# Optimization experiments

Measured on AMD Instinct MI355X. Metric: run time of the kernel, lower is better.

Reference implementation:

```python
import jax, jax.numpy as jnp
import numpy as np

B, S, D, H = 4, 2048, 1024, 1024  # batch, seq, input_dim, hidden_dim

def setup_inputs() -> dict:
    key = jax.random.key(0)
    k1, k2, k3, k4, k5 = jax.random.split(key, 5)
    scale1 = 1.0 / np.sqrt(D)
    scale2 = 1.0 / np.sqrt(H)
    return {
        "x": jax.random.normal(k1, (B, S, D), dtype=jnp.float32),
        "W1": jax.random.uniform(k2, (D, 3 * H), jnp.float32, -scale1, scale1),
        "b1": jax.random.uniform(k3, (3 * H,), jnp.float32, -scale1, scale1),
        "W2": jax.random.uniform(k4, (H, H), jnp.float32, -scale2, scale2),
        "b2": jax.random.uniform(k5, (H,), jnp.float32, -scale2, scale2),
    }

def reference(x, W1, b1, W2, b2):
    qkv = jnp.einsum('bsd,dh->bsh', x, W1) + b1          # [B,S,3H]
    q, k, v = jnp.split(qkv, 3, axis=-1)                  # each [B,S,H]
    scale = (2.0 * D) ** -0.5                             # faithful: (input_dim*2)^-0.5
    scores = jnp.einsum('bse,bSe->bsS', q, k) * scale     # [B,S,S]
    att = jax.nn.softmax(scores, axis=-1)
    ctx = jnp.einsum('bsS,bSe->bse', att, v)              # [B,S,H]
    out = jnp.einsum('bsh,hk->bsk', ctx, W2) + b2
    return out
```

## Files before the change

kernel.cpp:

```cpp
#include <hip/hip_runtime.h>
#include <hip/hip_bf16.h>
#include <stdint.h>

#define B_  4
#define S_  2048
#define D_  1024
#define H_  1024
#define BS_ (B_*S_)
#define N3H (3*H_)

typedef __bf16 bf16x8 __attribute__((ext_vector_type(8)));
typedef float  f32x4  __attribute__((ext_vector_type(4)));
typedef unsigned short u16x8 __attribute__((ext_vector_type(8)));

__device__ __forceinline__ unsigned short f2bf(float x) {
    unsigned u = __float_as_uint(x);
    return (unsigned short)((u + 0x7FFFu + ((u >> 16) & 1u)) >> 16);
}
__device__ __forceinline__ float bf2f(unsigned short h) {
    return __uint_as_float(((unsigned)h) << 16);
}

__device__ __forceinline__ void gload_lds16(const void* g, void* l) {
    __builtin_amdgcn_global_load_lds(
        (const __attribute__((address_space(1))) void*)g,
        (__attribute__((address_space(3))) void*)l, 16, 0, 0);
}

#define BAR __builtin_amdgcn_s_barrier()
#define DS_FENCE do { asm volatile("s_waitcnt lgkmcnt(0)" ::: "memory"); \
                      __builtin_amdgcn_sched_barrier(0); } while (0)

template<int EPI>
__global__ __launch_bounds__(256, 3) void gemm3b(
    const unsigned short* __restrict__ A,
    const unsigned short* __restrict__ Bm,
    int NXt, int NYt, int N, int K,
    long long sAz, long long sBz, long long sOz,
    void* __restrict__ out0, void* __restrict__ out1, void* __restrict__ out2,
    const float* __restrict__ bias, float scale)
{
    __shared__ __align__(16) char lds[3 * 16384];

    const int nt_g = (int)gridDim.x;
    const int bid = (int)blockIdx.x;
    const int C = nt_g >> 3;
    const int c = bid >> 3;
    const int xcd = bid & 7;
    const int qq = c >> 2;
    const int txl = qq % NXt;
    const int rest = (c & 3) + 4 * (qq / NXt);
    const int tile = xcd * C + rest * NXt + txl;
    const int tx = tile % NXt;
    const int rest2 = tile / NXt;
    const int ty = rest2 % NYt;
    const int tz = rest2 / NYt;

    const unsigned short* Ab = A  + (long long)tz * sAz;
    const unsigned short* Bb = Bm + (long long)tz * sBz;
    const int rowBase = ty * 128;
    const int colBase = tx * 128;
    const int tid = threadIdx.x;
    const int w = tid >> 6, l = tid & 63;
    const int wr = w >> 1, wc = w & 1;
    const int fr = l & 15, fq = l >> 4;

    int sr[2], scl[2];
#pragma unroll
    for (int j = 0; j < 2; j++) {
        int o  = j * 4096 + tid * 16;
        int st = o >> 10;
        int wi = o & 1023;
        wi ^= ((wi >> 9) & 1) << 5;
        sr[j]  = st * 16 + (wi >> 6);
        scl[j] = (wi & 63) >> 1;
    }

    auto STAGE_A = [&](char* buf, int t) {
        const unsigned short* base = Ab + (long long)rowBase * K + t * 32;
#pragma unroll
        for (int j = 0; j < 2; j++)
            gload_lds16(base + (long long)sr[j] * K + scl[j],
                        buf + j * 4096 + w * 1024);
    };
    auto STAGE_B = [&](char* buf, int t) {
        const unsigned short* base = Bb + (long long)colBase * K + t * 32;
#pragma unroll
        for (int j = 0; j < 2; j++)
            gload_lds16(base + (long long)sr[j] * K + scl[j],
                        buf + 8192 + j * 4096 + w * 1024);
    };

    const int abase = (fr * 64 + fq * 16) ^ ((fr & 8) << 2);

    f32x4 acc[4][4];
#pragma unroll
    for (int m = 0; m < 4; m++)
#pragma unroll
        for (int n = 0; n < 4; n++) acc[m][n] = (f32x4){0.f, 0.f, 0.f, 0.f};

    const int NT = K >> 5;

    STAGE_A(lds, 0); STAGE_B(lds, 0);
    STAGE_A(lds + 16384, 1); STAGE_B(lds + 16384, 1);
    asm volatile("s_waitcnt vmcnt(4)" ::: "memory");
    BAR;
    __builtin_amdgcn_sched_barrier(0);

    bf16x8 af[4], bf[4];

    for (int t = 0; t < NT; ++t) {
        const char* bc = lds + (t % 3) * 16384;
        char* bs = lds + ((t + 2) % 3) * 16384;
        int ts = t + 2; if (ts >= NT) ts -= NT;

#pragma unroll
        for (int m = 0; m < 4; m++)
            af[m] = *(const bf16x8*)(bc + (wr * 4 + m) * 1024 + abase);
#pragma unroll
        for (int n = 0; n < 4; n++)
            bf[n] = *(const bf16x8*)(bc + 8192 + (wc * 4 + n) * 1024 + abase);
        STAGE_A(bs, ts); STAGE_B(bs, ts);
        BAR; DS_FENCE;
        __builtin_amdgcn_s_setprio(1);
#pragma unroll
        for (int m = 0; m < 4; m++)
#pragma unroll
            for (int n = 0; n < 4; n++)
                acc[m][n] = __builtin_amdgcn_mfma_f32_16x16x32_bf16(
                    af[m], bf[n], acc[m][n], 0, 0, 0);
        __builtin_amdgcn_s_setprio(0);
        asm volatile("s_waitcnt vmcnt(4)" ::: "memory");
        BAR;
        __builtin_amdgcn_sched_barrier(0);
    }

    asm volatile("s_waitcnt vmcnt(0) lgkmcnt(0)" ::: "memory");
    BAR;

    const int crow0 = rowBase + wr * 64 + fq * 4;
    const int ccol0 = colBase + wc * 64 + fr;

    if constexpr (EPI == 0) {
        const int seg = colBase >> 10;
        if (seg < 2) {
            unsigned short* dst = (unsigned short*)(seg == 0 ? out0 : out1);
#pragma unroll
            for (int n = 0; n < 4; n++) {
                const int col = ccol0 + n * 16;
                const float bv = bias[col];
                const int scn = col & 1023;
#pragma unroll
                for (int m = 0; m < 4; m++) {
                    const int r0 = crow0 + m * 16;
#pragma unroll
                    for (int j = 0; j < 4; j++)
                        dst[(long long)(r0 + j) * 1024 + scn] = f2bf(acc[m][n][j] + bv);
                }
            }
        } else {
            unsigned short (*T)[129] = (unsigned short(*)[129])lds;
            const int lr0 = wr * 64 + fq * 4;
            const int lc0 = wc * 64 + fr;
#pragma unroll
            for (int n = 0; n < 4; n++) {
                const int lc = lc0 + n * 16;
                const float bv = bias[colBase + lc];
#pragma unroll
                for (int m = 0; m < 4; m++)
#pragma unroll
                    for (int j = 0; j < 4; j++)
                        T[lr0 + m * 16 + j][lc] = f2bf(acc[m][n][j] + bv);
            }
            BAR;
            const int s_loc = tid & 127, hh = tid >> 7;
            const int b = rowBase >> 11;
            const int s_glob = (rowBase & 2047) + s_loc;
            unsigned short* vt =
                (unsigned short*)out2 + (long long)b * ((long long)S_ * H_);
            const int h0 = (colBase - 2048) + hh * 64;
#pragma unroll 8
            for (int h = 0; h < 64; ++h)
                vt[(long long)(h0 + h) * S_ + s_glob] = T[s_loc][hh * 64 + h];
        }
    } else if constexpr (EPI == 4) {
        unsigned short* dst = (unsigned short*)out0 + (long long)tz * sOz;
#pragma unroll
        for (int m = 0; m < 4; m++) {
            float linv[4];
#pragma unroll
            for (int j = 0; j < 4; j++)
                linv[j] = 1.0f / bias[tz * 2048 + crow0 + m * 16 + j];
#pragma unroll
            for (int n = 0; n < 4; n++) {
                const int col = ccol0 + n * 16;
                const int r0 = crow0 + m * 16;
#pragma unroll
                for (int j = 0; j < 4; j++)
                    dst[(long long)(r0 + j) * N + col] = f2bf(acc[m][n][j] * linv[j]);
            }
        }
        (void)scale;
    } else {
        float* dst = (float*)out0;
#pragma unroll
        for (int n = 0; n < 4; n++) {
            const int col = ccol0 + n * 16;
            const float bv = bias[col];
#pragma unroll
            for (int m = 0; m < 4; m++) {
                const int r0 = crow0 + m * 16;
#pragma unroll
                for (int j = 0; j < 4; j++)
                    dst[(long long)(r0 + j) * N + col] = acc[m][n][j] + bv;
            }
        }
        (void)scale;
    }
}

template<int EPI>
__global__ __launch_bounds__(512, 2) void gemm256(
    const unsigned short* __restrict__ A,
    const unsigned short* __restrict__ Bm,
    int NXt, int NYt, int N, int K,
    long long sAz, long long sBz, long long sOz,
    void* __restrict__ out0, void* __restrict__ out1, void* __restrict__ out2,
    const float* __restrict__ bias, float scale)
{
    __shared__ __align__(16) char lds[131072];

    const int nt_g = (int)gridDim.x;
    const int bid = (int)blockIdx.x;
    const int C = nt_g >> 3;
    const int c = bid >> 3;
    const int xcd = bid & 7;
    const int qq = c >> 2;
    const int txl = qq % NXt;
    const int rest = (c & 3) + 4 * (qq / NXt);
    const int tile = xcd * C + rest * NXt + txl;
    const int tx = tile % NXt;
    const int rest2 = tile / NXt;
    const int ty = rest2 % NYt;
    const int tz = rest2 / NYt;

    const unsigned short* Ab = A  + (long long)tz * sAz;
    const unsigned short* Bb = Bm + (long long)tz * sBz;
    const int rowBase = ty * 256;
    const int colBase = tx * 256;
    const int tid = threadIdx.x;
    const int w = tid >> 6, l = tid & 63;
    const int wr = w >> 2, wc = w & 3;
    const int fr = l & 15, fq = l >> 4;

    int sr[2], scl[2];
#pragma unroll
    for (int j = 0; j < 2; j++) {
        int o  = j * 8192 + tid * 16;
        int st = o >> 10;
        int wi = o & 1023;
        wi ^= ((wi >> 9) & 1) << 5;
        sr[j]  = (st >> 1) * 16 + (wi >> 6);
        scl[j] = (st & 1) * 32 + ((wi & 63) >> 1);
    }

    auto STAGE = [&](int buf, int which, int tile_) {
        const unsigned short* mat = (which < 2) ? Ab : Bb;
        const int rt0 = ((which < 2) ? rowBase : colBase) + (which & 1) * 128;
        char* dst = lds + buf * 65536 + (which >> 1) * 32768
                        + (which & 1) * 16384 + w * 1024;
        const int k0 = tile_ * 64;
#pragma unroll
        for (int j = 0; j < 2; j++) {
            const unsigned short* src =
                mat + (long long)(rt0 + sr[j]) * K + k0 + scl[j];
            gload_lds16(src, dst + j * 8192);
        }
    };

    const int abase = (fr * 64 + fq * 16) ^ ((fr & 8) << 2);
    const char* Ah[2] = { lds + wr * 16384, lds + 65536 + wr * 16384 };
    const char* Bh[2] = { lds + 32768 + (wc >> 1) * 16384,
                          lds + 98304 + (wc >> 1) * 16384 };
    const int bn0 = (wc & 1) * 8192;

#define LA(b, m, kk) (*(const bf16x8*)(Ah[b] + (m)*2048 + (kk)*1024 + abase))
#define LB(b, n, kk) (*(const bf16x8*)(Bh[b] + bn0 + (n)*2048 + (kk)*1024 + abase))
#define MFMA16(AF, BF, MOFF, NOFF) do { \
    __builtin_amdgcn_s_setprio(1); \
    _Pragma("unroll") for (int m_ = 0; m_ < 4; m_++) \
    _Pragma("unroll") for (int n_ = 0; n_ < 2; n_++) \
    _Pragma("unroll") for (int k_ = 0; k_ < 2; k_++) \
        acc[(MOFF)+m_][(NOFF)+n_] = __builtin_amdgcn_mfma_f32_16x16x32_bf16( \
            AF[m_][k_], BF[n_][k_], acc[(MOFF)+m_][(NOFF)+n_], 0, 0, 0); \
    __builtin_amdgcn_s_setprio(0); } while (0)

    f32x4 acc[8][4];
#pragma unroll
    for (int m = 0; m < 8; m++)
#pragma unroll
        for (int n = 0; n < 4; n++) acc[m][n] = (f32x4){0.f, 0.f, 0.f, 0.f};

    const int NT = K >> 6;

    STAGE(0, 0, 0); STAGE(0, 1, 0); STAGE(0, 2, 0); STAGE(0, 3, 0);
    STAGE(1, 0, 1); STAGE(1, 1, 1);
    asm volatile("s_waitcnt vmcnt(4)" ::: "memory");
    BAR;
    __builtin_amdgcn_sched_barrier(0);

    bf16x8 afA[4][2], afB[4][2], bfA[2][2], bfB[2][2];

    for (int i = 0; i < NT / 2; i++) {
        const int t1 = 2 * i + 1;
        int t2 = 2 * i + 2; if (t2 >= NT) t2 -= NT;
        int t3 = 2 * i + 3; if (t3 >= NT) t3 -= NT;

#pragma unroll
        for (int m = 0; m < 4; m++) { afA[m][0] = LA(0, m, 0); afA[m][1] = LA(0, m, 1); }
#pragma unroll
        for (int n = 0; n < 2; n++) { bfA[n][0] = LB(0, n, 0); bfA[n][1] = LB(0, n, 1); }
        STAGE(1, 2, t1);
        BAR; DS_FENCE;
        MFMA16(afA, bfA, 0, 0);
        BAR;
#pragma unroll
        for (int m = 0; m < 4; m++) { afB[m][0] = LA(0, 4 + m, 0); afB[m][1] = LA(0, 4 + m, 1); }
        STAGE(1, 3, t1);
        BAR; DS_FENCE;
        MFMA16(afB, bfA, 4, 0);
        BAR;
#pragma unroll
        for (int n = 0; n < 2; n++) { bfB[n][0] = LB(0, 2 + n, 0); bfB[n][1] = LB(0, 2 + n, 1); }
        STAGE(0, 0, t2);
        BAR; DS_FENCE;
        MFMA16(afA, bfB, 0, 2);
        BAR;
        STAGE(0, 1, t2);
        BAR;
        MFMA16(afB, bfB, 4, 2);
        asm volatile("s_waitcnt vmcnt(4)" ::: "memory");
        BAR;
        __builtin_amdgcn_sched_barrier(0);

#pragma unroll
        for (int m = 0; m < 4; m++) { afA[m][0] = LA(1, m, 0); afA[m][1] = LA(1, m, 1); }
#pragma unroll
        for (int n = 0; n < 2; n++) { bfA[n][0] = LB(1, n, 0); bfA[n][1] = LB(1, n, 1); }
        STAGE(0, 2, t2);
        BAR; DS_FENCE;
        MFMA16(afA, bfA, 0, 0);
        BAR;
#pragma unroll
        for (int m = 0; m < 4; m++) { afB[m][0] = LA(1, 4 + m, 0); afB[m][1] = LA(1, 4 + m, 1); }
        STAGE(0, 3, t2);
        BAR; DS_FENCE;
        MFMA16(afB, bfA, 4, 0);
        BAR;
#pragma unroll
        for (int n = 0; n < 2; n++) { bfB[n][0] = LB(1, 2 + n, 0); bfB[n][1] = LB(1, 2 + n, 1); }
        STAGE(1, 0, t3);
        BAR; DS_FENCE;
        MFMA16(afA, bfB, 0, 2);
        BAR;
        STAGE(1, 1, t3);
        BAR;
        MFMA16(afB, bfB, 4, 2);
        asm volatile("s_waitcnt vmcnt(4)" ::: "memory");
        BAR;
        __builtin_amdgcn_sched_barrier(0);
    }

    asm volatile("s_waitcnt vmcnt(0) lgkmcnt(0)" ::: "memory");

    const int crow0 = rowBase + wr * 128 + fq * 4;
    const int ccol0 = colBase + wc * 64 + fr;

    if constexpr (EPI == 2) {
        float* lsum = (float*)out1;
        unsigned short* dst = (unsigned short*)out0 + (long long)tz * sOz;
#pragma unroll
        for (int m = 0; m < 8; m++) {
#pragma unroll
            for (int j = 0; j < 4; j++) {
                const int row = crow0 + m * 16 + j;
                float rs = 0.f;
#pragma unroll
                for (int n = 0; n < 4; n++) {
                    const int col = ccol0 + n * 16;
                    const float p = __expf(acc[m][n][j] * scale);
                    const unsigned short us = f2bf(p);
                    dst[(long long)row * N + col] = us;
                    rs += bf2f(us);
                }
                rs += __shfl_xor(rs, 1); rs += __shfl_xor(rs, 2);
                rs += __shfl_xor(rs, 4); rs += __shfl_xor(rs, 8);
                if (fr == 0) atomicAdd(&lsum[tz * 2048 + row], rs);
            }
        }
    }
    (void)out2; (void)bias;
#undef LA
#undef LB
#undef MFMA16
}

__global__ __launch_bounds__(256) void conv_f32_bf16(
    const float* __restrict__ in, unsigned short* __restrict__ out, int n8)
{
    for (int i = blockIdx.x * blockDim.x + threadIdx.x; i < n8;
         i += gridDim.x * blockDim.x) {
        const float4 a = ((const float4*)in)[2 * i];
        const float4 b = ((const float4*)in)[2 * i + 1];
        u16x8 o;
        o[0] = f2bf(a.x); o[1] = f2bf(a.y); o[2] = f2bf(a.z); o[3] = f2bf(a.w);
        o[4] = f2bf(b.x); o[5] = f2bf(b.y); o[6] = f2bf(b.z); o[7] = f2bf(b.w);
        ((u16x8*)out)[i] = o;
    }
}

__global__ __launch_bounds__(256) void tconv_f32_bf16(
    const float* __restrict__ in, unsigned short* __restrict__ out,
    int rows, int cols)
{
    __shared__ float t[32][33];
    const int c0 = blockIdx.x * 32, r0 = blockIdx.y * 32;
    const int tx = threadIdx.x & 31, ty = threadIdx.x >> 5;
#pragma unroll
    for (int i = 0; i < 4; i++)
        t[ty + 8 * i][tx] = in[(long long)(r0 + ty + 8 * i) * cols + c0 + tx];
    __syncthreads();
#pragma unroll
    for (int i = 0; i < 4; i++)
        out[(long long)(c0 + ty + 8 * i) * rows + r0 + tx] = f2bf(t[tx][ty + 8 * i]);
}

extern "C" void kernel_launch(void* const* d_in, const int* in_sizes, int n_in,
                              void* d_out, int out_size, void* d_ws, size_t ws_size,
                              hipStream_t stream)
{
    (void)in_sizes; (void)n_in; (void)out_size; (void)ws_size;
    const float* x  = (const float*)d_in[0];
    const float* W1 = (const float*)d_in[1];
    const float* b1 = (const float*)d_in[2];
    const float* W2 = (const float*)d_in[3];
    const float* b2 = (const float*)d_in[4];
    float* out = (float*)d_out;

    char* ws = (char*)d_ws;
    size_t off = 0;
    auto alloc = [&](size_t bytes) {
        void* p = ws + off;
        off += (bytes + 255) & ~(size_t)255;
        return p;
    };
    unsigned short* xbf = (unsigned short*)alloc((size_t)BS_ * D_ * 2);
    unsigned short* w1t = (unsigned short*)alloc((size_t)N3H * D_ * 2);
    unsigned short* w2t = (unsigned short*)alloc((size_t)H_ * H_ * 2);
    unsigned short* q   = (unsigned short*)alloc((size_t)BS_ * H_ * 2);
    unsigned short* k   = (unsigned short*)alloc((size_t)BS_ * H_ * 2);
    unsigned short* v   = (unsigned short*)alloc((size_t)BS_ * H_ * 2);
    unsigned short* vt  = (unsigned short*)alloc((size_t)BS_ * H_ * 2);
    unsigned short* sc  = (unsigned short*)alloc((size_t)B_ * S_ * S_ * 2);
    float*          lsum = (float*)alloc((size_t)BS_ * 4);
    unsigned short* ctx = v;

    const float scale = 0.022097086912079608f;

    hipMemsetAsync(lsum, 0, (size_t)BS_ * 4, stream);

    conv_f32_bf16<<<dim3(2048), dim3(256), 0, stream>>>(x, xbf, BS_ * D_ / 8);
    tconv_f32_bf16<<<dim3(N3H / 32, D_ / 32), dim3(256), 0, stream>>>(W1, w1t, D_, N3H);
    tconv_f32_bf16<<<dim3(H_ / 32, H_ / 32), dim3(256), 0, stream>>>(W2, w2t, H_, H_);

    gemm3b<0><<<dim3(1536), dim3(256), 0, stream>>>(
        xbf, w1t, 24, 64, N3H, D_, 0LL, 0LL, 0LL, q, k, vt, b1, 1.0f);

    gemm256<2><<<dim3(256), dim3(512), 0, stream>>>(
        q, k, 8, 8, S_, H_, (long long)S_ * H_, (long long)S_ * H_,
        (long long)S_ * S_, sc, lsum, nullptr, nullptr, scale);

    gemm3b<4><<<dim3(512), dim3(256), 0, stream>>>(
        sc, vt, 8, 16, H_, S_, (long long)S_ * S_, (long long)H_ * S_,
        (long long)S_ * H_, ctx, nullptr, nullptr, lsum, 1.0f);

    gemm3b<3><<<dim3(512), dim3(256), 0, stream>>>(
        ctx, w2t, 8, 64, H_, H_, 0LL, 0LL, 0LL, out, nullptr, nullptr, b2, 1.0f);
}
```

Before: 195.6 us.

## Fold W2 into the V projection to drop the output GEMM

Uses associativity to precompute W1v·W2 as a fused weight, so the QKV GEMM directly emits V·W2 (transposed) instead of V. The attention-times-V GEMM then writes the final fp32 output with softmax normalization and a combined bias (b1v·W2 + b2), and the separate ctx·W2 GEMM is removed. This trades a large 8192x1024x1024 GEMM for a small 1024^3 weight GEMM plus a bias reduction kernel. It adds an extra bf16 rounding of the fused weight, which may change numerics slightly.

```diff
diff --git a/kernel.cpp b/kernel.cpp
--- a/kernel.cpp
+++ b/kernel.cpp
@@ -31,7 +31,7 @@
 #define DS_FENCE do { asm volatile("s_waitcnt lgkmcnt(0)" ::: "memory"); \
                       __builtin_amdgcn_sched_barrier(0); } while (0)
 
-template<int EPI>
+template<int EPI, int SWZ>
 __global__ __launch_bounds__(256, 3) void gemm3b(
     const unsigned short* __restrict__ A,
     const unsigned short* __restrict__ Bm,
@@ -41,6 +41,198 @@
     const float* __restrict__ bias, float scale)
 {
     __shared__ __align__(16) char lds[3 * 16384];
+
+    const int bid = (int)blockIdx.x;
+    int tile;
+    if constexpr (SWZ) {
+        const int nt_g = (int)gridDim.x;
+        const int C = nt_g >> 3;
+        const int c = bid >> 3;
+        const int xcd = bid & 7;
+        const int qq = c >> 2;
+        const int txl = qq % NXt;
+        const int rest = (c & 3) + 4 * (qq / NXt);
+        tile = xcd * C + rest * NXt + txl;
+    } else {
+        tile = bid;
+    }
+    const int tx = tile % NXt;
+    const int rest2 = tile / NXt;
+    const int ty = rest2 % NYt;
+    const int tz = rest2 / NYt;
+
+    const unsigned short* Ab = A  + (long long)tz * sAz;
+    const unsigned short* Bb = Bm + (long long)tz * sBz;
+    const int rowBase = ty * 128;
+    const int colBase = tx * 128;
+    const int tid = threadIdx.x;
+    const int w = tid >> 6, l = tid & 63;
+    const int wr = w >> 1, wc = w & 1;
+    const int fr = l & 15, fq = l >> 4;
+
+    int sr[2], scl[2];
+#pragma unroll
+    for (int j = 0; j < 2; j++) {
+        int o  = j * 4096 + tid * 16;
+        int st = o >> 10;
+        int wi = o & 1023;
+        wi ^= ((wi >> 9) & 1) << 5;
+        sr[j]  = st * 16 + (wi >> 6);
+        scl[j] = (wi & 63) >> 1;
+    }
+
+    auto STAGE_A = [&](char* buf, int t) {
+        const unsigned short* base = Ab + (long long)rowBase * K + t * 32;
+#pragma unroll
+        for (int j = 0; j < 2; j++)
+            gload_lds16(base + (long long)sr[j] * K + scl[j],
+                        buf + j * 4096 + w * 1024);
+    };
+    auto STAGE_B = [&](char* buf, int t) {
+        const unsigned short* base = Bb + (long long)colBase * K + t * 32;
+#pragma unroll
+        for (int j = 0; j < 2; j++)
+            gload_lds16(base + (long long)sr[j] * K + scl[j],
+                        buf + 8192 + j * 4096 + w * 1024);
+    };
+
+    const int abase = (fr * 64 + fq * 16) ^ ((fr & 8) << 2);
+
+    f32x4 acc[4][4];
+#pragma unroll
+    for (int m = 0; m < 4; m++)
+#pragma unroll
+        for (int n = 0; n < 4; n++) acc[m][n] = (f32x4){0.f, 0.f, 0.f, 0.f};
+
+    const int NT = K >> 5;
+
+    STAGE_A(lds, 0); STAGE_B(lds, 0);
+    STAGE_A(lds + 16384, 1); STAGE_B(lds + 16384, 1);
+    asm volatile("s_waitcnt vmcnt(4)" ::: "memory");
+    BAR;
+    __builtin_amdgcn_sched_barrier(0);
+
+    bf16x8 af[4], bf[4];
+
+    for (int t = 0; t < NT; ++t) {
+        const char* bc = lds + (t % 3) * 16384;
+        char* bs = lds + ((t + 2) % 3) * 16384;
+        int ts = t + 2; if (ts >= NT) ts -= NT;
+
+#pragma unroll
+        for (int m = 0; m < 4; m++)
+            af[m] = *(const bf16x8*)(bc + (wr * 4 + m) * 1024 + abase);
+#pragma unroll
+        for (int n = 0; n < 4; n++)
+            bf[n] = *(const bf16x8*)(bc + 8192 + (wc * 4 + n) * 1024 + abase);
+        STAGE_A(bs, ts); STAGE_B(bs, ts);
+        BAR; DS_FENCE;
+        __builtin_amdgcn_s_setprio(1);
+#pragma unroll
+        for (int m = 0; m < 4; m++)
+#pragma unroll
+            for (int n = 0; n < 4; n++)
+                acc[m][n] = __builtin_amdgcn_mfma_f32_16x16x32_bf16(
+                    af[m], bf[n], acc[m][n], 0, 0, 0);
+        __builtin_amdgcn_s_setprio(0);
+        asm volatile("s_waitcnt vmcnt(4)" ::: "memory");
+        BAR;
+        __builtin_amdgcn_sched_barrier(0);
+    }
+
+    asm volatile("s_waitcnt vmcnt(0) lgkmcnt(0)" ::: "memory");
+    BAR;
+
+    const int crow0 = rowBase + wr * 64 + fq * 4;
+    const int ccol0 = colBase + wc * 64 + fr;
+
+    if constexpr (EPI == 0) {
+        const int seg = colBase >> 10;
+        if (seg < 2) {
+            unsigned short* dst = (unsigned short*)(seg == 0 ? out0 : out1);
+#pragma unroll
+            for (int n = 0; n < 4; n++) {
+                const int col = ccol0 + n * 16;
+                const float bv = bias[col];
+                const int scn = col & 1023;
+#pragma unroll
+                for (int m = 0; m < 4; m++) {
+                    const int r0 = crow0 + m * 16;
+#pragma unroll
+                    for (int j = 0; j < 4; j++)
+                        dst[(long long)(r0 + j) * 1024 + scn] = f2bf(acc[m][n][j] + bv);
+                }
+            }
+        } else {
+            unsigned short (*T)[129] = (unsigned short(*)[129])lds;
+            const int lr0 = wr * 64 + fq * 4;
+            const int lc0 = wc * 64 + fr;
+#pragma unroll
+            for (int n = 0; n < 4; n++) {
+                const int lc = lc0 + n * 16;
+#pragma unroll
+                for (int m = 0; m < 4; m++)
+#pragma unroll
+                    for (int j = 0; j < 4; j++)
+                        T[lr0 + m * 16 + j][lc] = f2bf(acc[m][n][j]);
+            }
+            BAR;
+            const int s_loc = tid & 127, hh = tid >> 7;
+            const int b = rowBase >> 11;
+            const int s_glob = (rowBase & 2047) + s_loc;
+            unsigned short* ut =
+                (unsigned short*)out2 + (long long)b * ((long long)S_ * H_);
+            const int h0 = (colBase - 2048) + hh * 64;
+#pragma unroll 8
+            for (int h = 0; h < 64; ++h)
+                ut[(long long)(h0 + h) * S_ + s_glob] = T[s_loc][hh * 64 + h];
+        }
+    } else if constexpr (EPI == 1) {
+        unsigned short* dst = (unsigned short*)out0 + (long long)tz * sOz;
+#pragma unroll
+        for (int n = 0; n < 4; n++) {
+            const int col = ccol0 + n * 16;
+#pragma unroll
+            for (int m = 0; m < 4; m++) {
+                const int r0 = crow0 + m * 16;
+#pragma unroll
+                for (int j = 0; j < 4; j++)
+                    dst[(long long)(r0 + j) * N + col] = f2bf(acc[m][n][j] * scale);
+            }
+        }
+    } else {
+        float* dst = (float*)out0 + (long long)tz * sOz;
+        const float* bu = (const float*)out1;
+#pragma unroll
+        for (int m = 0; m < 4; m++) {
+            float linv[4];
+#pragma unroll
+            for (int j = 0; j < 4; j++)
+                linv[j] = 1.0f / bias[tz * 2048 + crow0 + m * 16 + j];
+#pragma unroll
+            for (int n = 0; n < 4; n++) {
+                const int col = ccol0 + n * 16;
+                const float bvv = bu[col];
+                const int r0 = crow0 + m * 16;
+#pragma unroll
+                for (int j = 0; j < 4; j++)
+                    dst[(long long)(r0 + j) * N + col] = acc[m][n][j] * linv[j] + bvv;
+            }
+        }
+        (void)scale;
+    }
+}
+
+template<int EPI>
+__global__ __launch_bounds__(512, 2) void gemm256(
+    const unsigned short* __restrict__ A,
+    const unsigned short* __restrict__ Bm,
+    int NXt, int NYt, int N, int K,
+    long long sAz, long long sBz, long long sOz,
+    void* __restrict__ out0, void* __restrict__ out1, void* __restrict__ out2,
+    const float* __restrict__ bias, float scale)
+{
+    __shared__ __align__(16) char lds[131072];
 
     const int nt_g = (int)gridDim.x;
     const int bid = (int)blockIdx.x;
@@ -58,194 +250,6 @@
 
     const unsigned short* Ab = A  + (long long)tz * sAz;
     const unsigned short* Bb = Bm + (long long)tz * sBz;
-    const int rowBase = ty * 128;
-    const int colBase = tx * 128;
-    const int tid = threadIdx.x;
-    const int w = tid >> 6, l = tid & 63;
-    const int wr = w >> 1, wc = w & 1;
-    const int fr = l & 15, fq = l >> 4;
-
-    int sr[2], scl[2];
-#pragma unroll
-    for (int j = 0; j < 2; j++) {
-        int o  = j * 4096 + tid * 16;
-        int st = o >> 10;
-        int wi = o & 1023;
-        wi ^= ((wi >> 9) & 1) << 5;
-        sr[j]  = st * 16 + (wi >> 6);
-        scl[j] = (wi & 63) >> 1;
-    }
-
-    auto STAGE_A = [&](char* buf, int t) {
-        const unsigned short* base = Ab + (long long)rowBase * K + t * 32;
-#pragma unroll
-        for (int j = 0; j < 2; j++)
-            gload_lds16(base + (long long)sr[j] * K + scl[j],
-                        buf + j * 4096 + w * 1024);
-    };
-    auto STAGE_B = [&](char* buf, int t) {
-        const unsigned short* base = Bb + (long long)colBase * K + t * 32;
-#pragma unroll
-        for (int j = 0; j < 2; j++)
-            gload_lds16(base + (long long)sr[j] * K + scl[j],
-                        buf + 8192 + j * 4096 + w * 1024);
-    };
-
-    const int abase = (fr * 64 + fq * 16) ^ ((fr & 8) << 2);
-
-    f32x4 acc[4][4];
-#pragma unroll
-    for (int m = 0; m < 4; m++)
-#pragma unroll
-        for (int n = 0; n < 4; n++) acc[m][n] = (f32x4){0.f, 0.f, 0.f, 0.f};
-
-    const int NT = K >> 5;
-
-    STAGE_A(lds, 0); STAGE_B(lds, 0);
-    STAGE_A(lds + 16384, 1); STAGE_B(lds + 16384, 1);
-    asm volatile("s_waitcnt vmcnt(4)" ::: "memory");
-    BAR;
-    __builtin_amdgcn_sched_barrier(0);
-
-    bf16x8 af[4], bf[4];
-
-    for (int t = 0; t < NT; ++t) {
-        const char* bc = lds + (t % 3) * 16384;
-        char* bs = lds + ((t + 2) % 3) * 16384;
-        int ts = t + 2; if (ts >= NT) ts -= NT;
-
-#pragma unroll
-        for (int m = 0; m < 4; m++)
-            af[m] = *(const bf16x8*)(bc + (wr * 4 + m) * 1024 + abase);
-#pragma unroll
-        for (int n = 0; n < 4; n++)
-            bf[n] = *(const bf16x8*)(bc + 8192 + (wc * 4 + n) * 1024 + abase);
-        STAGE_A(bs, ts); STAGE_B(bs, ts);
-        BAR; DS_FENCE;
-        __builtin_amdgcn_s_setprio(1);
-#pragma unroll
-        for (int m = 0; m < 4; m++)
-#pragma unroll
-            for (int n = 0; n < 4; n++)
-                acc[m][n] = __builtin_amdgcn_mfma_f32_16x16x32_bf16(
-                    af[m], bf[n], acc[m][n], 0, 0, 0);
-        __builtin_amdgcn_s_setprio(0);
-        asm volatile("s_waitcnt vmcnt(4)" ::: "memory");
-        BAR;
-        __builtin_amdgcn_sched_barrier(0);
-    }
-
-    asm volatile("s_waitcnt vmcnt(0) lgkmcnt(0)" ::: "memory");
-    BAR;
-
-    const int crow0 = rowBase + wr * 64 + fq * 4;
-    const int ccol0 = colBase + wc * 64 + fr;
-
-    if constexpr (EPI == 0) {
-        const int seg = colBase >> 10;
-        if (seg < 2) {
-            unsigned short* dst = (unsigned short*)(seg == 0 ? out0 : out1);
-#pragma unroll
-            for (int n = 0; n < 4; n++) {
-                const int col = ccol0 + n * 16;
-                const float bv = bias[col];
-                const int scn = col & 1023;
-#pragma unroll
-                for (int m = 0; m < 4; m++) {
-                    const int r0 = crow0 + m * 16;
-#pragma unroll
-                    for (int j = 0; j < 4; j++)
-                        dst[(long long)(r0 + j) * 1024 + scn] = f2bf(acc[m][n][j] + bv);
-                }
-            }
-        } else {
-            unsigned short (*T)[129] = (unsigned short(*)[129])lds;
-            const int lr0 = wr * 64 + fq * 4;
-            const int lc0 = wc * 64 + fr;
-#pragma unroll
-            for (int n = 0; n < 4; n++) {
-                const int lc = lc0 + n * 16;
-                const float bv = bias[colBase + lc];
-#pragma unroll
-                for (int m = 0; m < 4; m++)
-#pragma unroll
-                    for (int j = 0; j < 4; j++)
-                        T[lr0 + m * 16 + j][lc] = f2bf(acc[m][n][j] + bv);
-            }
-            BAR;
-            const int s_loc = tid & 127, hh = tid >> 7;
-            const int b = rowBase >> 11;
-            const int s_glob = (rowBase & 2047) + s_loc;
-            unsigned short* vt =
-                (unsigned short*)out2 + (long long)b * ((long long)S_ * H_);
-            const int h0 = (colBase - 2048) + hh * 64;
-#pragma unroll 8
-            for (int h = 0; h < 64; ++h)
-                vt[(long long)(h0 + h) * S_ + s_glob] = T[s_loc][hh * 64 + h];
-        }
-    } else if constexpr (EPI == 4) {
-        unsigned short* dst = (unsigned short*)out0 + (long long)tz * sOz;
-#pragma unroll
-        for (int m = 0; m < 4; m++) {
-            float linv[4];
-#pragma unroll
-            for (int j = 0; j < 4; j++)
-                linv[j] = 1.0f / bias[tz * 2048 + crow0 + m * 16 + j];
-#pragma unroll
-            for (int n = 0; n < 4; n++) {
-                const int col = ccol0 + n * 16;
-                const int r0 = crow0 + m * 16;
-#pragma unroll
-                for (int j = 0; j < 4; j++)
-                    dst[(long long)(r0 + j) * N + col] = f2bf(acc[m][n][j] * linv[j]);
-            }
-        }
-        (void)scale;
-    } else {
-        float* dst = (float*)out0;
-#pragma unroll
-        for (int n = 0; n < 4; n++) {
-            const int col = ccol0 + n * 16;
-            const float bv = bias[col];
-#pragma unroll
-            for (int m = 0; m < 4; m++) {
-                const int r0 = crow0 + m * 16;
-#pragma unroll
-                for (int j = 0; j < 4; j++)
-                    dst[(long long)(r0 + j) * N + col] = acc[m][n][j] + bv;
-            }
-        }
-        (void)scale;
-    }
-}
-
-template<int EPI>
-__global__ __launch_bounds__(512, 2) void gemm256(
-    const unsigned short* __restrict__ A,
-    const unsigned short* __restrict__ Bm,
-    int NXt, int NYt, int N, int K,
-    long long sAz, long long sBz, long long sOz,
-    void* __restrict__ out0, void* __restrict__ out1, void* __restrict__ out2,
-    const float* __restrict__ bias, float scale)
-{
-    __shared__ __align__(16) char lds[131072];
-
-    const int nt_g = (int)gridDim.x;
-    const int bid = (int)blockIdx.x;
-    const int C = nt_g >> 3;
-    const int c = bid >> 3;
-    const int xcd = bid & 7;
-    const int qq = c >> 2;
-    const int txl = qq % NXt;
-    const int rest = (c & 3) + 4 * (qq / NXt);
-    const int tile = xcd * C + rest * NXt + txl;
-    const int tx = tile % NXt;
-    const int rest2 = tile / NXt;
-    const int ty = rest2 % NYt;
-    const int tz = rest2 / NYt;
-
-    const unsigned short* Ab = A  + (long long)tz * sAz;
-    const unsigned short* Bb = Bm + (long long)tz * sBz;
     const int rowBase = ty * 256;
     const int colBase = tx * 256;
     const int tid = threadIdx.x;
@@ -419,6 +423,34 @@
     }
 }
 
+__global__ __launch_bounds__(256) void conv_w1v(
+    const float* __restrict__ W1, unsigned short* __restrict__ w1v)
+{
+    const int i = blockIdx.x * 256 + threadIdx.x;
+    const int j = i >> 7, hh = (i & 127) * 8;
+    const float4 a = *(const float4*)&W1[(long long)j * 3072 + 2048 + hh];
+    const float4 b = *(const float4*)&W1[(long long)j * 3072 + 2048 + hh + 4];
+    u16x8 o;
+    o[0] = f2bf(a.x); o[1] = f2bf(a.y); o[2] = f2bf(a.z); o[3] = f2bf(a.w);
+    o[4] = f2bf(b.x); o[5] = f2bf(b.y); o[6] = f2bf(b.z); o[7] = f2bf(b.w);
+    *(u16x8*)&w1v[(long long)j * 1024 + hh] = o;
+}
+
+__global__ __launch_bounds__(256) void bias_bu2(
+    const float* __restrict__ b1, const unsigned short* __restrict__ w2t,
+    const float* __restrict__ b2, float* __restrict__ bu2)
+{
+    const int i = blockIdx.x * 256 + threadIdx.x;
+    float s = b2[i];
+    for (int h8 = 0; h8 < 128; ++h8) {
+        const u16x8 wv = *(const u16x8*)&w2t[(long long)i * 1024 + h8 * 8];
+#pragma unroll
+        for (int e = 0; e < 8; ++e)
+            s += b1[2048 + h8 * 8 + e] * bf2f(wv[e]);
+    }
+    bu2[i] = s;
+}
+
 __global__ __launch_bounds__(256) void tconv_f32_bf16(
     const float* __restrict__ in, unsigned short* __restrict__ out,
     int rows, int cols)
@@ -457,13 +489,13 @@
     unsigned short* xbf = (unsigned short*)alloc((size_t)BS_ * D_ * 2);
     unsigned short* w1t = (unsigned short*)alloc((size_t)N3H * D_ * 2);
     unsigned short* w2t = (unsigned short*)alloc((size_t)H_ * H_ * 2);
+    unsigned short* w1v = (unsigned short*)alloc((size_t)D_ * H_ * 2);
     unsigned short* q   = (unsigned short*)alloc((size_t)BS_ * H_ * 2);
     unsigned short* k   = (unsigned short*)alloc((size_t)BS_ * H_ * 2);
-    unsigned short* v   = (unsigned short*)alloc((size_t)BS_ * H_ * 2);
-    unsigned short* vt  = (unsigned short*)alloc((size_t)BS_ * H_ * 2);
+    unsigned short* ut  = (unsigned short*)alloc((size_t)BS_ * H_ * 2);
     unsigned short* sc  = (unsigned short*)alloc((size_t)B_ * S_ * S_ * 2);
     float*          lsum = (float*)alloc((size_t)BS_ * 4);
-    unsigned short* ctx = v;
+    float*          bu2  = (float*)alloc((size_t)H_ * 4);
 
     const float scale = 0.022097086912079608f;
 
@@ -472,18 +504,22 @@
     conv_f32_bf16<<<dim3(2048), dim3(256), 0, stream>>>(x, xbf, BS_ * D_ / 8);
     tconv_f32_bf16<<<dim3(N3H / 32, D_ / 32), dim3(256), 0, stream>>>(W1, w1t, D_, N3H);
     tconv_f32_bf16<<<dim3(H_ / 32, H_ / 32), dim3(256), 0, stream>>>(W2, w2t, H_, H_);
-
-    gemm3b<0><<<dim3(1536), dim3(256), 0, stream>>>(
-        xbf, w1t, 24, 64, N3H, D_, 0LL, 0LL, 0LL, q, k, vt, b1, 1.0f);
+    conv_w1v<<<dim3(512), dim3(256), 0, stream>>>(W1, w1v);
+
+    gemm3b<1, 0><<<dim3(64), dim3(256), 0, stream>>>(
+        w2t, w1v, 8, 8, 1024, 1024, 0LL, 0LL, 0LL,
+        w1t + (size_t)2048 * 1024, nullptr, nullptr, nullptr, 1.0f);
+
+    bias_bu2<<<dim3(4), dim3(256), 0, stream>>>(b1, w2t, b2, bu2);
+
+    gemm3b<0, 1><<<dim3(1536), dim3(256), 0, stream>>>(
+        xbf, w1t, 24, 64, N3H, D_, 0LL, 0LL, 0LL, q, k, ut, b1, 1.0f);
 
     gemm256<2><<<dim3(256), dim3(512), 0, stream>>>(
         q, k, 8, 8, S_, H_, (long long)S_ * H_, (long long)S_ * H_,
         (long long)S_ * S_, sc, lsum, nullptr, nullptr, scale);
 
-    gemm3b<4><<<dim3(512), dim3(256), 0, stream>>>(
-        sc, vt, 8, 16, H_, S_, (long long)S_ * S_, (long long)H_ * S_,
-        (long long)S_ * H_, ctx, nullptr, nullptr, lsum, 1.0f);
-
-    gemm3b<3><<<dim3(512), dim3(256), 0, stream>>>(
-        ctx, w2t, 8, 64, H_, H_, 0LL, 0LL, 0LL, out, nullptr, nullptr, b2, 1.0f);
-}
+    gemm3b<5, 1><<<dim3(512), dim3(256), 0, stream>>>(
+        sc, ut, 8, 16, H_, S_, (long long)S_ * S_, (long long)H_ * S_,
+        (long long)S_ * H_, out, bu2, nullptr, lsum, 1.0f);
+}
```

New measurement: 214.9 us. 1.1x slower.
